# Performance work log

Measured on AMD Instinct MI355X. Metric: run time of the kernel, lower is better.

The kernel has to match this reference:

```python
import jax, jax.numpy as jnp
import numpy as np

HID = 128
NB = 50000   # base nodes
NC = 2500    # centroid nodes
L = 2        # conv layers
EDGES = {'bb': 800000, 'bc': 200000, 'cc': 40000, 'cb': 200000}
SIZES = {'bb': (NB, NB), 'bc': (NB, NC), 'cc': (NC, NC), 'cb': (NC, NB)}


def gelu(x):
    return jax.nn.gelu(x, approximate=False)  # torch F.gelu default is exact erf


def setup_inputs() -> dict:
    key = jax.random.key(0)
    ks = iter(jax.random.split(key, 64))
    def n(shape, s=1.0):
        return jax.random.normal(next(ks), shape, jnp.float32) * s
    inp = {}
    inp['x_base'] = n((NB, HID))
    inp['x_cent'] = n((NC, HID))
    for t, (ns, nd) in SIZES.items():
        e = EDGES[t]
        src = jax.random.randint(next(ks), (e,), 0, ns)
        dst = jax.random.randint(next(ks), (e,), 0, nd)
        inp[f'ei_{t}'] = jnp.stack([src, dst])          # [2, E]
        inp[f'ea_{t}'] = n((e, HID))                     # edge attributes
        inp[f'ew_{t}'] = jax.random.uniform(next(ks), (e,), jnp.float32)
    # stacked per-(layer, edge_type) parameters; edge type order: 0=bb 1=bc 2=cc 3=cb
    s = 0.05
    inp['Wsrc'] = n((L, 4, HID, HID), s); inp['bsrc'] = jnp.zeros((L, 4, HID))
    inp['Wdst'] = n((L, 4, HID, HID), s); inp['bdst'] = jnp.zeros((L, 4, HID))
    inp['eps']  = jnp.zeros((L, 4))   # GINE eps, init 0 as in module
    inp['We']   = n((L, 4, HID, HID), s); inp['be']  = jnp.zeros((L, 4, HID))
    inp['Wm1']  = n((L, 4, HID, HID), s); inp['bm1'] = jnp.zeros((L, 4, HID))
    inp['Wm2']  = n((L, 4, HID, HID), s); inp['bm2'] = jnp.zeros((L, 4, HID))
    return inp


def _gine_conv(x_src, x_dst, ei, ea, ew, Ws, bs, Wd, bd, eps, We, be, W1, b1, W2, b2):
    src, dst = ei[0], ei[1]
    xs = x_src @ Ws + bs                         # lin_src
    e = ea @ We + be                             # edge_encoder
    m = gelu(xs[src] + e) * ew[:, None]          # message: gather -> gelu -> scale
    agg = jax.ops.segment_sum(m, dst, num_segments=x_dst.shape[0])  # aggr='add'
    h = agg + ((1.0 + eps) * x_dst) @ Wd + bd    # (1+eps)*x_dst -> lin_dst, add
    return gelu(h @ W1 + b1) @ W2 + b2           # MLP [hid, hid, hid]


def _forward(x_base, x_cent, ei_bb, ei_bc, ei_cc, ei_cb,
             ea_bb, ea_bc, ea_cc, ea_cb, ew_bb, ew_bc, ew_cc, ew_cb,
             Wsrc, bsrc, Wdst, bdst, eps, We, be, Wm1, bm1, Wm2, bm2):
    def p(l, t):
        return (Wsrc[l, t], bsrc[l, t], Wdst[l, t], bdst[l, t], eps[l, t],
                We[l, t], be[l, t], Wm1[l, t], bm1[l, t], Wm2[l, t], bm2[l, t])
    xb, xc = x_base, x_cent
    for l in range(L):
        # all 4 relations at the same rank (parallel=True); HeteroConv aggr='sum' per dst
        ob = _gine_conv(xb, xb, ei_bb, ea_bb, ew_bb, *p(l, 0)) \
           + _gine_conv(xc, xb, ei_cb, ea_cb, ew_cb, *p(l, 3))
        oc = _gine_conv(xb, xc, ei_bc, ea_bc, ew_bc, *p(l, 1)) \
           + _gine_conv(xc, xc, ei_cc, ea_cc, ew_cc, *p(l, 2))
        xb = xb + gelu(ob)   # use_res=True; dropout p=0 / eval -> no-op
        xc = xc + gelu(oc)
    return xb, xc


def reference(x_base, x_cent, ei_bb, ei_bc, ei_cc, ei_cb,
              ea_bb, ea_bc, ea_cc, ea_cb, ew_bb, ew_bc, ew_cc, ew_cb,
              Wsrc, bsrc, Wdst, bdst, eps, We, be, Wm1, bm1, Wm2, bm2):
    return _forward(x_base, x_cent, ei_bb, ei_bc, ei_cc, ei_cb,
                    ea_bb, ea_bc, ea_cc, ea_cb, ew_bb, ew_bc, ew_cc, ew_cb,
                    Wsrc, bsrc, Wdst, bdst, eps, We, be, Wm1, bm1, Wm2, bm2)
```

## Files before the change

### kernel.cpp

```cpp
#include <hip/hip_runtime.h>
#include <hip/hip_bf16.h>

#define LDSK 136

typedef __bf16 bf16x8_t __attribute__((ext_vector_type(8)));
typedef float  f32x4_t  __attribute__((ext_vector_type(4)));

__device__ __forceinline__ float gelu_f(float x) {
    return 0.5f * x * (1.0f + erff(x * 0.70710678118654752440f));
}

__device__ __forceinline__ void stage_w_bias(const float* __restrict__ W,
                                             const float* __restrict__ bvec,
                                             __bf16* Wt, float* bias_s) {
    for (int i = threadIdx.x * 8; i < 128 * 128; i += 256 * 8) {
        int k = i >> 7, n = i & 127;
        f32x4_t v0 = *(const f32x4_t*)(W + i);
        f32x4_t v1 = *(const f32x4_t*)(W + i + 4);
        #pragma unroll
        for (int j = 0; j < 4; ++j) {
            Wt[(n + j) * LDSK + k]     = (__bf16)v0[j];
            Wt[(n + 4 + j) * LDSK + k] = (__bf16)v1[j];
        }
    }
    if (threadIdx.x < 128) bias_s[threadIdx.x] = bvec[threadIdx.x];
}

__global__ __launch_bounds__(256) void k_node_gemm(
    const float* __restrict__ A, int M,
    const float* __restrict__ W, const float* __restrict__ bvec,
    const float* __restrict__ eps_elem,
    const float* __restrict__ ADD, float* __restrict__ OUT,
    int do_gelu, int accum)
{
    __shared__ __bf16 Wt[128 * LDSK];
    __shared__ float bias_s[128];
    stage_w_bias(W, bvec, Wt, bias_s);
    __syncthreads();

    int lane = threadIdx.x & 63, wave = threadIdx.x >> 6;
    int q = lane >> 4, c = lane & 15;
    int m0 = blockIdx.x * 64 + wave * 16;

    float ascale = 1.0f;
    if (eps_elem) ascale = 1.0f + *eps_elem;

    int arow = m0 + c;
    bf16x8_t afr[4];
    if (arow < M) {
        const float* ap = A + (size_t)arow * 128;
        #pragma unroll
        for (int kb = 0; kb < 4; ++kb) {
            const float* p = ap + kb * 32 + q * 8;
            f32x4_t x0 = *(const f32x4_t*)p;
            f32x4_t x1 = *(const f32x4_t*)(p + 4);
            bf16x8_t v;
            #pragma unroll
            for (int j = 0; j < 4; ++j) {
                v[j]     = (__bf16)(x0[j] * ascale);
                v[j + 4] = (__bf16)(x1[j] * ascale);
            }
            afr[kb] = v;
        }
    } else {
        #pragma unroll
        for (int kb = 0; kb < 4; ++kb) {
            bf16x8_t z;
            #pragma unroll
            for (int j = 0; j < 8; ++j) z[j] = (__bf16)0.0f;
            afr[kb] = z;
        }
    }

    #pragma unroll
    for (int nt = 0; nt < 8; ++nt) {
        f32x4_t acc = {0.f, 0.f, 0.f, 0.f};
        #pragma unroll
        for (int kb = 0; kb < 4; ++kb) {
            bf16x8_t b = *(const bf16x8_t*)&Wt[(nt * 16 + c) * LDSK + kb * 32 + q * 8];
            acc = __builtin_amdgcn_mfma_f32_16x16x32_bf16(afr[kb], b, acc, 0, 0, 0);
        }
        int col = nt * 16 + c;
        #pragma unroll
        for (int r = 0; r < 4; ++r) {
            int rowg = m0 + q * 4 + r;
            if (rowg < M) {
                size_t o = (size_t)rowg * 128 + col;
                float v = acc[r] + bias_s[col];
                if (ADD) v += ADD[o];
                if (do_gelu) v = gelu_f(v);
                if (accum) v += OUT[o];
                OUT[o] = v;
            }
        }
    }
}

__global__ __launch_bounds__(256) void k_edge(
    const float* __restrict__ ea,
    const int* __restrict__ esrc, const int* __restrict__ edst,
    const float* __restrict__ ew, int E,
    const float* __restrict__ W, const float* __restrict__ bvec,
    const float* __restrict__ XS, float* __restrict__ AGG)
{
    __shared__ __bf16 Wt[128 * LDSK];
    __shared__ float bias_s[128];
    stage_w_bias(W, bvec, Wt, bias_s);
    __syncthreads();

    int lane = threadIdx.x & 63, wave = threadIdx.x >> 6;
    int q = lane >> 4, c = lane & 15;
    int m0 = blockIdx.x * 64 + wave * 16;

    const float* ap = ea + (size_t)(m0 + c) * 128;
    bf16x8_t afr[4];
    #pragma unroll
    for (int kb = 0; kb < 4; ++kb) {
        const float* p = ap + kb * 32 + q * 8;
        f32x4_t x0 = *(const f32x4_t*)p;
        f32x4_t x1 = *(const f32x4_t*)(p + 4);
        bf16x8_t v;
        #pragma unroll
        for (int j = 0; j < 4; ++j) {
            v[j]     = (__bf16)x0[j];
            v[j + 4] = (__bf16)x1[j];
        }
        afr[kb] = v;
    }

    int se[4], de[4];
    float wv[4];
    #pragma unroll
    for (int r = 0; r < 4; ++r) {
        int e = m0 + q * 4 + r;
        se[r] = esrc[e];
        de[r] = edst[e];
        wv[r] = ew[e];
    }

    #pragma unroll
    for (int nt = 0; nt < 8; ++nt) {
        f32x4_t acc = {0.f, 0.f, 0.f, 0.f};
        #pragma unroll
        for (int kb = 0; kb < 4; ++kb) {
            bf16x8_t b = *(const bf16x8_t*)&Wt[(nt * 16 + c) * LDSK + kb * 32 + q * 8];
            acc = __builtin_amdgcn_mfma_f32_16x16x32_bf16(afr[kb], b, acc, 0, 0, 0);
        }
        int col = nt * 16 + c;
        #pragma unroll
        for (int r = 0; r < 4; ++r) {
            float v = acc[r] + bias_s[col] + XS[(size_t)se[r] * 128 + col];
            v = gelu_f(v) * wv[r];
            atomicAdd(&AGG[(size_t)de[r] * 128 + col], v);
        }
    }
}

__global__ void k_copy(const float* __restrict__ in, float* __restrict__ out, int n) {
    int i = blockIdx.x * 256 + threadIdx.x;
    if (i < n) out[i] = in[i];
}

__global__ void k_zero(float* __restrict__ p, int n) {
    int i = blockIdx.x * 256 + threadIdx.x;
    if (i < n) p[i] = 0.0f;
}

__global__ void k_residual(float* __restrict__ X, const float* __restrict__ O, int n) {
    int i = blockIdx.x * 256 + threadIdx.x;
    if (i < n) X[i] += gelu_f(O[i]);
}

__global__ void k_store(const float* __restrict__ XB, const float* __restrict__ XC,
                        float* __restrict__ out, int nb, int nc) {
    int i = blockIdx.x * 256 + threadIdx.x;
    if (i < nb) out[i] = XB[i];
    else if (i < nb + nc) out[i] = XC[i - nb];
}

extern "C" void kernel_launch(void* const* d_in, const int* in_sizes, int n_in,
                              void* d_out, int out_size, void* d_ws, size_t ws_size,
                              hipStream_t stream)
{
    const float* xb_in = (const float*)d_in[0];
    const float* xc_in = (const float*)d_in[1];
    const int NB = in_sizes[0] / 128;
    const int NC = in_sizes[1] / 128;

    const int slot[4] = {2, 5, 8, 11};
    const int* ei_[4]; const float *ea_[4], *ew_[4]; int E_[4];
    for (int t = 0; t < 4; ++t) {
        ei_[t] = (const int*)d_in[slot[t]];
        ea_[t] = (const float*)d_in[slot[t] + 1];
        ew_[t] = (const float*)d_in[slot[t] + 2];
        E_[t]  = in_sizes[slot[t]] / 2;
    }
    const float* Wsrc = (const float*)d_in[14];
    const float* bsrc = (const float*)d_in[15];
    const float* Wdst = (const float*)d_in[16];
    const float* bdst = (const float*)d_in[17];
    const float* epsp = (const float*)d_in[18];
    const float* Wep  = (const float*)d_in[19];
    const float* bep  = (const float*)d_in[20];
    const float* Wm1  = (const float*)d_in[21];
    const float* bm1  = (const float*)d_in[22];
    const float* Wm2  = (const float*)d_in[23];
    const float* bm2  = (const float*)d_in[24];

    float* XB  = (float*)d_ws;
    float* XC  = XB  + (size_t)NB * 128;
    float* XS  = XC  + (size_t)NC * 128;
    float* AGG = XS  + (size_t)NB * 128;
    float* T   = AGG;
    float* OB  = AGG + (size_t)NB * 128;
    float* OC  = OB  + (size_t)NB * 128;

    dim3 blk(256);
    k_copy<<<dim3((NB * 128 + 255) / 256), blk, 0, stream>>>(xb_in, XB, NB * 128);
    k_copy<<<dim3((NC * 128 + 255) / 256), blk, 0, stream>>>(xc_in, XC, NC * 128);

    const int tlist[4] = {0, 3, 1, 2};
    for (int l = 0; l < 2; ++l) {
        for (int bi = 0; bi < 4; ++bi) {
            int t = tlist[bi];
            const float* srcx = (t == 0 || t == 1) ? XB : XC;
            int ns            = (t == 0 || t == 1) ? NB : NC;
            const float* dstx = (t == 0 || t == 3) ? XB : XC;
            int nd            = (t == 0 || t == 3) ? NB : NC;
            float* outp       = (t == 0 || t == 3) ? OB : OC;
            int accum         = (bi == 1 || bi == 3);
            size_t pi = (size_t)(l * 4 + t);

            k_node_gemm<<<dim3((ns + 63) / 64), blk, 0, stream>>>(
                srcx, ns, Wsrc + pi * 16384, bsrc + pi * 128,
                nullptr, nullptr, XS, 0, 0);
            int nz = nd * 128;
            k_zero<<<dim3((nz + 255) / 256), blk, 0, stream>>>(AGG, nz);
            int E = E_[t];
            k_edge<<<dim3(E / 64), blk, 0, stream>>>(
                ea_[t], ei_[t], ei_[t] + E, ew_[t], E,
                Wep + pi * 16384, bep + pi * 128, XS, AGG);
            k_node_gemm<<<dim3((nd + 63) / 64), blk, 0, stream>>>(
                dstx, nd, Wdst + pi * 16384, bdst + pi * 128,
                epsp + pi, AGG, XS, 0, 0);
            k_node_gemm<<<dim3((nd + 63) / 64), blk, 0, stream>>>(
                XS, nd, Wm1 + pi * 16384, bm1 + pi * 128,
                nullptr, nullptr, T, 1, 0);
            k_node_gemm<<<dim3((nd + 63) / 64), blk, 0, stream>>>(
                T, nd, Wm2 + pi * 16384, bm2 + pi * 128,
                nullptr, nullptr, outp, 0, accum);
        }
        k_residual<<<dim3((NB * 128 + 255) / 256), blk, 0, stream>>>(XB, OB, NB * 128);
        k_residual<<<dim3((NC * 128 + 255) / 256), blk, 0, stream>>>(XC, OC, NC * 128);
    }
    k_store<<<dim3((out_size + 255) / 256), blk, 0, stream>>>(
        XB, XC, (float*)d_out, NB * 128, NC * 128);
}
```

Measured before the change: 2.703 ms.

## Sort edges by destination and pre-reduce messages before atomic scatter

Adds a per-call counting sort of each edge type by destination (histogram, exclusive scan, scatter) producing permuted src/dst/weight arrays. The edge kernel reads edges in sorted order, swaps MFMA operands so each lane owns four consecutive columns of one edge, and performs a segmented shuffle reduction across lanes with equal destination so only segment heads issue atomics. This targets atomic contention and scattered XS gathers, at the cost of extra preprocessing kernels, a single-block scan, and gathered edge-attribute reads.

```diff
diff --git a/kernel.cpp b/kernel.cpp
--- a/kernel.cpp
+++ b/kernel.cpp
@@ -33,8 +33,8 @@
     const float* __restrict__ ADD, float* __restrict__ OUT,
     int do_gelu, int accum)
 {
-    __shared__ __bf16 Wt[128 * LDSK];
-    __shared__ float bias_s[128];
+    __shared__ __align__(16) __bf16 Wt[128 * LDSK];
+    __shared__ __align__(16) float bias_s[128];
     stage_w_bias(W, bvec, Wt, bias_s);
     __syncthreads();
 
@@ -96,23 +96,79 @@
     }
 }
 
+
+__global__ void k_zero_i(int* __restrict__ p, int n) {
+    int i = blockIdx.x * 256 + threadIdx.x;
+    if (i < n) p[i] = 0;
+}
+
+__global__ void k_hist(const int* __restrict__ dst, int E, int* __restrict__ cnt) {
+    int i = blockIdx.x * 256 + threadIdx.x;
+    if (i < E) atomicAdd(&cnt[dst[i]], 1);
+}
+
+__global__ __launch_bounds__(1024) void k_scan_excl(const int* __restrict__ cnt,
+                                                    int* __restrict__ off, int n) {
+    __shared__ int sm[1024];
+    __shared__ int carry;
+    int tid = threadIdx.x;
+    if (tid == 0) carry = 0;
+    __syncthreads();
+    for (int base = 0; base < n; base += 1024) {
+        int i = base + tid;
+        int v = (i < n) ? cnt[i] : 0;
+        sm[tid] = v;
+        __syncthreads();
+        for (int o = 1; o < 1024; o <<= 1) {
+            int t = (tid >= o) ? sm[tid - o] : 0;
+            __syncthreads();
+            sm[tid] += t;
+            __syncthreads();
+        }
+        if (i < n) off[i] = carry + sm[tid] - v;
+        int total = sm[1023];
+        __syncthreads();
+        if (tid == 0) carry += total;
+        __syncthreads();
+    }
+}
+
+__global__ void k_scatter(const int* __restrict__ src, const int* __restrict__ dst,
+                          const float* __restrict__ ew, int E,
+                          int* __restrict__ off, int* __restrict__ perm,
+                          int* __restrict__ sse, int* __restrict__ sde,
+                          float* __restrict__ sew) {
+    int e = blockIdx.x * 256 + threadIdx.x;
+    if (e < E) {
+        int d = dst[e];
+        int p = atomicAdd(&off[d], 1);
+        perm[p] = e;
+        sse[p]  = src[e];
+        sde[p]  = d;
+        sew[p]  = ew[e];
+    }
+}
+
 __global__ __launch_bounds__(256) void k_edge(
     const float* __restrict__ ea,
-    const int* __restrict__ esrc, const int* __restrict__ edst,
-    const float* __restrict__ ew, int E,
+    const int* __restrict__ perm,
+    const int* __restrict__ sse, const int* __restrict__ sde,
+    const float* __restrict__ sew, int E,
     const float* __restrict__ W, const float* __restrict__ bvec,
     const float* __restrict__ XS, float* __restrict__ AGG)
 {
-    __shared__ __bf16 Wt[128 * LDSK];
-    __shared__ float bias_s[128];
+    __shared__ __align__(16) __bf16 Wt[128 * LDSK];
+    __shared__ __align__(16) float bias_s[128];
     stage_w_bias(W, bvec, Wt, bias_s);
     __syncthreads();
 
     int lane = threadIdx.x & 63, wave = threadIdx.x >> 6;
     int q = lane >> 4, c = lane & 15;
     int m0 = blockIdx.x * 64 + wave * 16;
-
-    const float* ap = ea + (size_t)(m0 + c) * 128;
+    int es = m0 + c;
+
+    int pe = perm[es];
+    const float* ap = ea + (size_t)pe * 128;
     bf16x8_t afr[4];
     #pragma unroll
     for (int kb = 0; kb < 4; ++kb) {
@@ -128,15 +184,19 @@
         afr[kb] = v;
     }
 
-    int se[4], de[4];
-    float wv[4];
-    #pragma unroll
-    for (int r = 0; r < 4; ++r) {
-        int e = m0 + q * 4 + r;
-        se[r] = esrc[e];
-        de[r] = edst[e];
-        wv[r] = ew[e];
-    }
+    int se   = sse[es];
+    int de   = sde[es];
+    float wv = sew[es];
+    const float* xsp = XS + (size_t)se * 128;
+    float* aggp      = AGG + (size_t)de * 128;
+
+    int dnb;
+    dnb = __shfl(de, lane + 1); bool s1 = (c + 1 < 16) && (dnb == de);
+    dnb = __shfl(de, lane + 2); bool s2 = (c + 2 < 16) && (dnb == de);
+    dnb = __shfl(de, lane + 4); bool s4 = (c + 4 < 16) && (dnb == de);
+    dnb = __shfl(de, lane + 8); bool s8 = (c + 8 < 16) && (dnb == de);
+    int dprev = __shfl(de, lane - 1);
+    bool head = (c == 0) || (dprev != de);
 
     #pragma unroll
     for (int nt = 0; nt < 8; ++nt) {
@@ -144,14 +204,35 @@
         #pragma unroll
         for (int kb = 0; kb < 4; ++kb) {
             bf16x8_t b = *(const bf16x8_t*)&Wt[(nt * 16 + c) * LDSK + kb * 32 + q * 8];
-            acc = __builtin_amdgcn_mfma_f32_16x16x32_bf16(afr[kb], b, acc, 0, 0, 0);
-        }
-        int col = nt * 16 + c;
-        #pragma unroll
-        for (int r = 0; r < 4; ++r) {
-            float v = acc[r] + bias_s[col] + XS[(size_t)se[r] * 128 + col];
-            v = gelu_f(v) * wv[r];
-            atomicAdd(&AGG[(size_t)de[r] * 128 + col], v);
+            acc = __builtin_amdgcn_mfma_f32_16x16x32_bf16(b, afr[kb], acc, 0, 0, 0);
+        }
+        int col0 = nt * 16 + q * 4;
+        f32x4_t xs4 = *(const f32x4_t*)(xsp + col0);
+        f32x4_t b4  = *(const f32x4_t*)(bias_s + col0);
+        float v0 = gelu_f(acc[0] + b4[0] + xs4[0]) * wv;
+        float v1 = gelu_f(acc[1] + b4[1] + xs4[1]) * wv;
+        float v2 = gelu_f(acc[2] + b4[2] + xs4[2]) * wv;
+        float v3 = gelu_f(acc[3] + b4[3] + xs4[3]) * wv;
+
+        float n0, n1, n2, n3;
+        n0 = __shfl_down(v0, 1); n1 = __shfl_down(v1, 1);
+        n2 = __shfl_down(v2, 1); n3 = __shfl_down(v3, 1);
+        if (s1) { v0 += n0; v1 += n1; v2 += n2; v3 += n3; }
+        n0 = __shfl_down(v0, 2); n1 = __shfl_down(v1, 2);
+        n2 = __shfl_down(v2, 2); n3 = __shfl_down(v3, 2);
+        if (s2) { v0 += n0; v1 += n1; v2 += n2; v3 += n3; }
+        n0 = __shfl_down(v0, 4); n1 = __shfl_down(v1, 4);
+        n2 = __shfl_down(v2, 4); n3 = __shfl_down(v3, 4);
+        if (s4) { v0 += n0; v1 += n1; v2 += n2; v3 += n3; }
+        n0 = __shfl_down(v0, 8); n1 = __shfl_down(v1, 8);
+        n2 = __shfl_down(v2, 8); n3 = __shfl_down(v3, 8);
+        if (s8) { v0 += n0; v1 += n1; v2 += n2; v3 += n3; }
+
+        if (head) {
+            atomicAdd(aggp + col0 + 0, v0);
+            atomicAdd(aggp + col0 + 1, v1);
+            atomicAdd(aggp + col0 + 2, v2);
+            atomicAdd(aggp + col0 + 3, v3);
         }
     }
 }
@@ -215,9 +296,33 @@
     float* OB  = AGG + (size_t)NB * 128;
     float* OC  = OB  + (size_t)NB * 128;
 
+    int* ip = (int*)(OC + (size_t)NC * 128);
+    int *PERM[4], *SSE[4], *SDE[4], *CNT[4], *OFF[4];
+    float* SEW[4];
+    const int nd_[4] = {NB, NC, NC, NB};
+    for (int t = 0; t < 4; ++t) {
+        int E = E_[t];
+        PERM[t] = ip; ip += E;
+        SSE[t]  = ip; ip += E;
+        SDE[t]  = ip; ip += E;
+        SEW[t]  = (float*)ip; ip += E;
+        CNT[t]  = ip; ip += nd_[t];
+        OFF[t]  = ip; ip += nd_[t];
+    }
+
     dim3 blk(256);
     k_copy<<<dim3((NB * 128 + 255) / 256), blk, 0, stream>>>(xb_in, XB, NB * 128);
     k_copy<<<dim3((NC * 128 + 255) / 256), blk, 0, stream>>>(xc_in, XC, NC * 128);
+
+    for (int t = 0; t < 4; ++t) {
+        int E = E_[t], nd = nd_[t];
+        const int* dstp = ei_[t] + E;
+        k_zero_i<<<dim3((nd + 255) / 256), blk, 0, stream>>>(CNT[t], nd);
+        k_hist<<<dim3((E + 255) / 256), blk, 0, stream>>>(dstp, E, CNT[t]);
+        k_scan_excl<<<dim3(1), dim3(1024), 0, stream>>>(CNT[t], OFF[t], nd);
+        k_scatter<<<dim3((E + 255) / 256), blk, 0, stream>>>(
+            ei_[t], dstp, ew_[t], E, OFF[t], PERM[t], SSE[t], SDE[t], SEW[t]);
+    }
 
     const int tlist[4] = {0, 3, 1, 2};
     for (int l = 0; l < 2; ++l) {
@@ -238,7 +343,7 @@
             k_zero<<<dim3((nz + 255) / 256), blk, 0, stream>>>(AGG, nz);
             int E = E_[t];
             k_edge<<<dim3(E / 64), blk, 0, stream>>>(
-                ea_[t], ei_[t], ei_[t] + E, ew_[t], E,
+                ea_[t], PERM[t], SSE[t], SDE[t], SEW[t], E,
                 Wep + pi * 16384, bep + pi * 128, XS, AGG);
             k_node_gemm<<<dim3((nd + 63) / 64), blk, 0, stream>>>(
                 dstx, nd, Wdst + pi * 16384, bdst + pi * 128,
```

After: 2.957 ms. 1.09x slower.
